# Kernel optimization log

Measured on AMD Instinct MI355X. Metric: run time of the kernel, lower is better.

The kernel has to match this reference:

```python
import math
import jax, jax.numpy as jnp
import numpy as np


def _cirlen(scale):
    # replicates UpSample.get_cirlen: smallest rational period of the scale
    for i in (10, 100, 1000, 10000):
        y = scale * i
        x = i
        if y == math.floor(y):
            break
    y = int(round(y))
    g = math.gcd(x, y)
    return y // g


def _proj(out_len, scale, scale_int, in_len):
    # replicates matmask_made: for each output coord, source coord and repeat index (sca),
    # giving the selected column p = coord*scale_int + sca in the nearest-repeated grid.
    c = np.arange(out_len, dtype=np.float64)
    c[-1] -= 0.1
    coord = np.floor(c / scale).astype(np.int64)
    sca = np.arange(out_len) - np.searchsorted(coord, coord)  # occurrence index per coord
    p = coord * scale_int + sca
    # unfold(kernel=3, dilation=2, padding=2): taps at p-2, p, p+2 in the upscaled grid
    q = p[:, None] + 2 * np.array([-1, 0, 1], dtype=np.int64)[None, :]
    valid = ((q >= 0) & (q < in_len * scale_int)).astype(np.float32)
    src = np.clip(q // scale_int, 0, in_len - 1)  # upscaled pixel q == original pixel q//scale_int
    return src, valid


def reference(x, w1, b1, w2, b2, ln_g, ln_b, scale_x10):
    scale = round(scale_x10 / 10.0, 4)
    scale_int = math.ceil(scale)
    N, C, H, W = x.shape
    outH = math.ceil(scale * H)
    outW = math.ceil(scale * W)
    cycle = _cirlen(scale)
    K = 9 * C

    # ---- per-cycle-position dynamic weights (Scale2Pos_mat + Fea2Weight + LayerNorm) ----
    off = np.arange(cycle, dtype=np.float64) / scale
    off = (off - np.floor(off)).astype(np.float32)
    oh_i, ow_j = np.meshgrid(off, off, indexing='ij')  # row index = i*cycle + j
    posmat = np.stack([np.full_like(oh_i, 1.0 / scale), oh_i, ow_j], axis=-1).reshape(-1, 3)
    posmat = jnp.asarray(posmat)
    h = jax.nn.relu(posmat @ w1 + b1)                       # (cyc^2, 256)
    wflat = h @ w2 + b2                                     # (cyc^2, 9*C*outC)
    outC = wflat.shape[-1] // K
    wv = wflat.reshape(cycle * cycle, outC, K)              # view(pos, outC, K)
    mu = wv.mean(-1, keepdims=True)
    var = wv.var(-1, keepdims=True)                         # biased, as torch LayerNorm
    wv = ((wv - mu) / jnp.sqrt(var + 1e-5)) * ln_g + ln_b
    wv = wv / C
    Wm = jnp.transpose(wv, (0, 2, 1)).reshape(cycle, cycle, K, outC)

    # ---- irregular gather (nearest-repeat + unfold + mask_select), done as direct gather ----
    rs, vh = _proj(outH, scale, scale_int, H)  # (outH,3)
    cs, vw = _proj(outW, scale, scale_int, W)  # (outW,3)
    g = x[:, :, jnp.asarray(rs), :]            # (N,C,outH,3,W)
    g = g[:, :, :, :, jnp.asarray(cs)]         # (N,C,outH,3,outW,3)
    g = g * jnp.asarray(vh)[None, None, :, :, None, None]
    g = g * jnp.asarray(vw)[None, None, None, None, :, :]
    # unfold channel order is (C, kh, kw)
    patch = jnp.transpose(g, (0, 2, 4, 1, 3, 5)).reshape(N, outH, outW, K)

    # ---- pad to cycle multiple, per-cycle-position matmul, crop ----
    Hp = -(-outH // cycle) * cycle
    Wp = -(-outW // cycle) * cycle
    patch = jnp.pad(patch, ((0, 0), (0, Hp - outH), (0, Wp - outW), (0, 0)))
    patch = patch.reshape(N, Hp // cycle, cycle, Wp // cycle, cycle, K)
    out = jnp.einsum('nhiwjk,ijkc->nchiwj', patch, Wm)
    out = out.reshape(N, outC, Hp, Wp)[:, :, :outH, :outW]
    return out


def setup_inputs() -> dict:
    key = jax.random.key(0)
    k = jax.random.split(key, 5)
    inC, outC = 64, 3
    x = jax.random.normal(k[0], (8, inC, 96, 96), dtype=jnp.float32)
    w1 = jax.random.normal(k[1], (3, 256), dtype=jnp.float32) * 0.5
    b1 = jax.random.normal(k[2], (256,), dtype=jnp.float32) * 0.1
    w2 = jax.random.normal(k[3], (256, 9 * inC * outC), dtype=jnp.float32) * 0.0625
    b2 = jax.random.normal(k[4], (9 * inC * outC,), dtype=jnp.float32) * 0.01
    ln_g = jnp.ones((9 * inC,), dtype=jnp.float32)
    ln_b = jnp.zeros((9 * inC,), dtype=jnp.float32)
    return {"x": x, "w1": w1, "b1": b1, "w2": w2, "b2": b2,
            "ln_g": ln_g, "ln_b": ln_b, "scale_x10": 15}
```

## Files before the change

kernel.cpp:

```cpp
#include <hip/hip_runtime.h>
#include <math.h>

#define C_IN   64
#define HW_IN  96
#define N_B    8
#define OUTC   3
#define OUT_HW 144
#define HID    256
#define KDIM   576
#define NFLAT  1728

#define WS_W    0
#define WS_RS   15552
#define WS_VH   15984
#define WS_WF   16416

__global__ __launch_bounds__(256) void a1_wflat(
    const float* __restrict__ w1, const float* __restrict__ b1,
    const float* __restrict__ w2, const float* __restrict__ b2,
    const int* __restrict__ sxp, float* __restrict__ ws)
{
    __shared__ float h[HID];
    __shared__ float part[4 * 64];
    const int cell = blockIdx.x;
    const int tile = blockIdx.y;
    const int tid  = threadIdx.x;

    double scale = (double)sxp[0] / 10.0;
    int ci = cell / 3, cj = cell % 3;
    double oi = (double)ci / scale; oi -= floor(oi);
    double oj = (double)cj / scale; oj -= floor(oj);
    float p0 = (float)(1.0 / scale), p1 = (float)oi, p2 = (float)oj;

    float hv = b1[tid] + p0 * w1[tid] + p1 * w1[HID + tid] + p2 * w1[2 * HID + tid];
    h[tid] = fmaxf(hv, 0.f);
    __syncthreads();

    const int wave = tid >> 6, lane = tid & 63;
    const int col  = tile * 64 + lane;
    const float* w2c = w2 + (size_t)(wave * 64) * NFLAT + col;
    const float* hp  = h + wave * 64;
    float v = 0.f;
    #pragma unroll
    for (int r = 0; r < 64; ++r) v += hp[r] * w2c[(size_t)r * NFLAT];
    part[wave * 64 + lane] = v;
    __syncthreads();

    if (tid < 64) {
        int c2 = tile * 64 + tid;
        float s = b2[c2] + part[tid] + part[64 + tid] + part[128 + tid] + part[192 + tid];
        ws[WS_WF + cell * NFLAT + c2] = s;
    }
}

__global__ __launch_bounds__(256) void a2_ln_pack_proj(
    const float* __restrict__ ln_g, const float* __restrict__ ln_b,
    const int* __restrict__ sxp, float* __restrict__ ws)
{
    __shared__ float rsum[4], rsum2[4];
    const int cell = blockIdx.x, co = blockIdx.y, tid = threadIdx.x;
    const int lane = tid & 63, wid = tid >> 6;

    const float* wfc = ws + WS_WF + cell * NFLAT + co * KDIM;

    float s = 0.f, s2 = 0.f;
    for (int k = tid; k < KDIM; k += 256) { float v = wfc[k]; s += v; s2 += v * v; }
    #pragma unroll
    for (int off = 32; off > 0; off >>= 1) { s += __shfl_down(s, off); s2 += __shfl_down(s2, off); }
    if (lane == 0) { rsum[wid] = s; rsum2[wid] = s2; }
    __syncthreads();
    float S  = rsum[0] + rsum[1] + rsum[2] + rsum[3];
    float Q  = rsum2[0] + rsum2[1] + rsum2[2] + rsum2[3];
    float mu = S * (1.f / KDIM);
    float rstd = rsqrtf(Q * (1.f / KDIM) - mu * mu + 1e-5f);

    for (int k = tid; k < KDIM; k += 256) {
        float v = ((wfc[k] - mu) * rstd * ln_g[k] + ln_b[k]) * (1.f / C_IN);
        int c = k / 9, t = k % 9;
        ws[WS_W + cell * NFLAT + c * 27 + t * 3 + co] = v;
    }

    if (cell == 0 && co == 0 && tid < OUT_HW) {
        double scale = (double)sxp[0] / 10.0;
        int scale_int = (int)ceil(scale - 1e-9);
        double cc = (double)tid; if (tid == OUT_HW - 1) cc -= 0.1;
        long coord = (long)floor(cc / scale);
        long first = (long)ceil((double)coord * scale);
        long p = coord * (long)scale_int + ((long)tid - first);
        #pragma unroll
        for (int d = 0; d < 3; ++d) {
            long q = p + 2 * (d - 1);
            bool ok = (q >= 0) && (q < (long)HW_IN * scale_int);
            long src = (q < 0) ? 0 : q / scale_int;
            if (src > HW_IN - 1) src = HW_IN - 1;
            ws[WS_RS + tid * 3 + d] = (float)src;
            ws[WS_VH + tid * 3 + d] = ok ? 1.f : 0.f;
        }
    }
}

#define JSTRIDE 2056

__global__ __launch_bounds__(192) void c_main(
    const float* __restrict__ x, const float* __restrict__ ws,
    float* __restrict__ out)
{
    __shared__ float Wl[3 * JSTRIDE];
    const int tid = threadIdx.x;
    const int oh  = blockIdx.x;
    const int n0  = blockIdx.y;
    const int i   = oh % 3;

    for (int idx = tid; idx < 3 * 64 * 32; idx += 192) {
        int j = idx >> 11;
        int rem = idx & 2047;
        int c = rem >> 5, m = rem & 31;
        float v = 0.f;
        if (m < 27) v = ws[WS_W + (size_t)((i * 3 + j) * 64 + c) * 27 + m];
        Wl[j * JSTRIDE + c * 32 + m] = v;
    }
    __syncthreads();

    const int ow = tid;
    if (ow >= OUT_HW) return;

    const float* rsf = ws + WS_RS;
    const float* vhf = ws + WS_VH;
    const int jj = ow % 3;
    const float* Wj = Wl + jj * JSTRIDE;

    int s[3]; float vw[3];
    #pragma unroll
    for (int d = 0; d < 3; ++d) { s[d] = (int)rsf[ow * 3 + d]; vw[d] = vhf[ow * 3 + d]; }

    int xoff[9]; float vv[9];
    #pragma unroll
    for (int dr = 0; dr < 3; ++dr) {
        int r = (int)rsf[oh * 3 + dr];
        float vhd = vhf[oh * 3 + dr];
        #pragma unroll
        for (int dc = 0; dc < 3; ++dc) {
            xoff[dr * 3 + dc] = r * HW_IN + s[dc];
            vv[dr * 3 + dc]   = vhd * vw[dc];
        }
    }

    const float* xb0 = x + (size_t)n0 * C_IN * HW_IN * HW_IN;
    const float* xb1 = xb0 + (size_t)4 * C_IN * HW_IN * HW_IN;
    float acc[2][3] = {{0.f,0.f,0.f},{0.f,0.f,0.f}};

    #pragma unroll 2
    for (int c = 0; c < C_IN; ++c) {
        const float* xc0 = xb0 + c * (HW_IN * HW_IN);
        const float* xc1 = xb1 + c * (HW_IN * HW_IN);
        float w[28];
        const float4* wp = (const float4*)(Wj + c * 32);
        #pragma unroll
        for (int q = 0; q < 7; ++q) ((float4*)w)[q] = wp[q];
        #pragma unroll
        for (int t = 0; t < 9; ++t) {
            float xv0 = xc0[xoff[t]] * vv[t];
            float xv1 = xc1[xoff[t]] * vv[t];
            acc[0][0] += xv0 * w[t * 3 + 0];
            acc[0][1] += xv0 * w[t * 3 + 1];
            acc[0][2] += xv0 * w[t * 3 + 2];
            acc[1][0] += xv1 * w[t * 3 + 0];
            acc[1][1] += xv1 * w[t * 3 + 1];
            acc[1][2] += xv1 * w[t * 3 + 2];
        }
    }

    #pragma unroll
    for (int rr = 0; rr < 2; ++rr) {
        int n = n0 + rr * 4;
        #pragma unroll
        for (int co = 0; co < OUTC; ++co)
            out[((size_t)(n * OUTC + co) * OUT_HW + oh) * OUT_HW + ow] = acc[rr][co];
    }
}

extern "C" void kernel_launch(void* const* d_in, const int* in_sizes, int n_in,
                              void* d_out, int out_size, void* d_ws, size_t ws_size,
                              hipStream_t stream)
{
    const float* x    = (const float*)d_in[0];
    const float* w1   = (const float*)d_in[1];
    const float* b1   = (const float*)d_in[2];
    const float* w2   = (const float*)d_in[3];
    const float* b2   = (const float*)d_in[4];
    const float* ln_g = (const float*)d_in[5];
    const float* ln_b = (const float*)d_in[6];
    const int*   sx   = (const int*)d_in[7];
    float* ws  = (float*)d_ws;
    float* out = (float*)d_out;

    a1_wflat<<<dim3(9, 27), 256, 0, stream>>>(w1, b1, w2, b2, sx, ws);
    a2_ln_pack_proj<<<dim3(9, 3), 256, 0, stream>>>(ln_g, ln_b, sx, ws);
    c_main<<<dim3(OUT_HW, 4), 192, 0, stream>>>(x, ws, out);
}
```

Before: 137.8 us.

## Regroup main kernel by cycle phase so each block shares uniform weights

```diff
diff --git a/kernel.cpp b/kernel.cpp
--- a/kernel.cpp
+++ b/kernel.cpp
@@ -99,84 +99,84 @@
     }
 }
 
-#define JSTRIDE 2056
-
-__global__ __launch_bounds__(192) void c_main(
+__global__ __launch_bounds__(256) void c_phase(
     const float* __restrict__ x, const float* __restrict__ ws,
     float* __restrict__ out)
 {
-    __shared__ float Wl[3 * JSTRIDE];
-    const int tid = threadIdx.x;
-    const int oh  = blockIdx.x;
-    const int n0  = blockIdx.y;
-    const int i   = oh % 3;
-
-    for (int idx = tid; idx < 3 * 64 * 32; idx += 192) {
-        int j = idx >> 11;
-        int rem = idx & 2047;
-        int c = rem >> 5, m = rem & 31;
-        float v = 0.f;
-        if (m < 27) v = ws[WS_W + (size_t)((i * 3 + j) * 64 + c) * 27 + m];
-        Wl[j * JSTRIDE + c * 32 + m] = v;
-    }
-    __syncthreads();
-
-    const int ow = tid;
-    if (ow >= OUT_HW) return;
+    const int tid   = threadIdx.x;
+    const int phase = blockIdx.y;
+    const int i  = phase / 3, jj = phase % 3;
+    const int idx = blockIdx.x * 256 + tid;
+    const int ow_idx = idx % 48;
+    const int t2     = idx / 48;
+    const int oh_idx = t2 % 48;
+    const int n      = t2 / 48;
+    const int oh = i  + 3 * oh_idx;
+    const int ow = jj + 3 * ow_idx;
 
     const float* rsf = ws + WS_RS;
     const float* vhf = ws + WS_VH;
-    const int jj = ow % 3;
-    const float* Wj = Wl + jj * JSTRIDE;
 
     int s[3]; float vw[3];
     #pragma unroll
     for (int d = 0; d < 3; ++d) { s[d] = (int)rsf[ow * 3 + d]; vw[d] = vhf[ow * 3 + d]; }
 
-    int xoff[9]; float vv[9];
+    int xoff[9]; float vv[9]; bool interior = true;
     #pragma unroll
     for (int dr = 0; dr < 3; ++dr) {
         int r = (int)rsf[oh * 3 + dr];
         float vhd = vhf[oh * 3 + dr];
         #pragma unroll
         for (int dc = 0; dc < 3; ++dc) {
+            float v = vhd * vw[dc];
             xoff[dr * 3 + dc] = r * HW_IN + s[dc];
-            vv[dr * 3 + dc]   = vhd * vw[dc];
-        }
-    }
-
-    const float* xb0 = x + (size_t)n0 * C_IN * HW_IN * HW_IN;
-    const float* xb1 = xb0 + (size_t)4 * C_IN * HW_IN * HW_IN;
-    float acc[2][3] = {{0.f,0.f,0.f},{0.f,0.f,0.f}};
-
-    #pragma unroll 2
-    for (int c = 0; c < C_IN; ++c) {
-        const float* xc0 = xb0 + c * (HW_IN * HW_IN);
-        const float* xc1 = xb1 + c * (HW_IN * HW_IN);
-        float w[28];
-        const float4* wp = (const float4*)(Wj + c * 32);
-        #pragma unroll
-        for (int q = 0; q < 7; ++q) ((float4*)w)[q] = wp[q];
-        #pragma unroll
-        for (int t = 0; t < 9; ++t) {
-            float xv0 = xc0[xoff[t]] * vv[t];
-            float xv1 = xc1[xoff[t]] * vv[t];
-            acc[0][0] += xv0 * w[t * 3 + 0];
-            acc[0][1] += xv0 * w[t * 3 + 1];
-            acc[0][2] += xv0 * w[t * 3 + 2];
-            acc[1][0] += xv1 * w[t * 3 + 0];
-            acc[1][1] += xv1 * w[t * 3 + 1];
-            acc[1][2] += xv1 * w[t * 3 + 2];
-        }
-    }
-
-    #pragma unroll
-    for (int rr = 0; rr < 2; ++rr) {
-        int n = n0 + rr * 4;
-        #pragma unroll
-        for (int co = 0; co < OUTC; ++co)
-            out[((size_t)(n * OUTC + co) * OUT_HW + oh) * OUT_HW + ow] = acc[rr][co];
-    }
+            vv[dr * 3 + dc]   = v;
+            interior = interior && (v == 1.f);
+        }
+    }
+
+    const float* wcell = ws + WS_W + phase * NFLAT;
+    const float* xc = x + (size_t)n * C_IN * (HW_IN * HW_IN);
+    float a0 = 0.f, a1 = 0.f, a2 = 0.f;
+
+    if (interior) {
+        #pragma unroll 2
+        for (int c = 0; c < C_IN; ++c) {
+            const float* wp = wcell + c * 27;
+            float w[27];
+            #pragma unroll
+            for (int q = 0; q < 27; ++q) w[q] = wp[q];
+            #pragma unroll
+            for (int t = 0; t < 9; ++t) {
+                float xv = xc[xoff[t]];
+                a0 += xv * w[t * 3 + 0];
+                a1 += xv * w[t * 3 + 1];
+                a2 += xv * w[t * 3 + 2];
+            }
+            xc += HW_IN * HW_IN;
+        }
+    } else {
+        #pragma unroll 2
+        for (int c = 0; c < C_IN; ++c) {
+            const float* wp = wcell + c * 27;
+            float w[27];
+            #pragma unroll
+            for (int q = 0; q < 27; ++q) w[q] = wp[q];
+            #pragma unroll
+            for (int t = 0; t < 9; ++t) {
+                float xv = xc[xoff[t]] * vv[t];
+                a0 += xv * w[t * 3 + 0];
+                a1 += xv * w[t * 3 + 1];
+                a2 += xv * w[t * 3 + 2];
+            }
+            xc += HW_IN * HW_IN;
+        }
+    }
+
+    const size_t ob = ((size_t)n * OUTC) * (OUT_HW * OUT_HW) + (size_t)oh * OUT_HW + ow;
+    out[ob]                           = a0;
+    out[ob +     (OUT_HW * OUT_HW)]   = a1;
+    out[ob + 2 * (OUT_HW * OUT_HW)]   = a2;
 }
 
 extern "C" void kernel_launch(void* const* d_in, const int* in_sizes, int n_in,
@@ -196,5 +196,5 @@
 
     a1_wflat<<<dim3(9, 27), 256, 0, stream>>>(w1, b1, w2, b2, sx, ws);
     a2_ln_pack_proj<<<dim3(9, 3), 256, 0, stream>>>(ln_g, ln_b, sx, ws);
-    c_main<<<dim3(OUT_HW, 4), 192, 0, stream>>>(x, ws, out);
-}
+    c_phase<<<dim3(72, 9), 256, 0, stream>>>(x, ws, out);
+}
```

Measured after the change: 160.9 us. 1.17x slower.

## Recast upsample conv as per-phase bf16 MFMA GEMM over padded NHWC input

Applied to the files above, without the earlier changes.

```diff
diff --git a/kernel.cpp b/kernel.cpp
--- a/kernel.cpp
+++ b/kernel.cpp
@@ -10,15 +10,29 @@
 #define KDIM   576
 #define NFLAT  1728
 
+typedef __attribute__((ext_vector_type(8))) short short8;
+typedef __attribute__((ext_vector_type(4))) float f32x4;
+
+#define XP_BYTES   (8u * 98 * 98 * 64 * 2)
+#define WP_OFF     XP_BYTES
+#define WF_OFF     (WP_OFF + 9 * 9216 * 2)
+#define WS_NEED    (WF_OFF + NFLAT * 9 * 4)
+
 #define WS_W    0
 #define WS_RS   15552
 #define WS_VH   15984
 #define WS_WF   16416
 
+__device__ __forceinline__ short f2bf(float f) {
+    unsigned u = __float_as_uint(f);
+    u += 0x7FFFu + ((u >> 16) & 1u);
+    return (short)(u >> 16);
+}
+
 __global__ __launch_bounds__(256) void a1_wflat(
     const float* __restrict__ w1, const float* __restrict__ b1,
     const float* __restrict__ w2, const float* __restrict__ b2,
-    const int* __restrict__ sxp, float* __restrict__ ws)
+    const int* __restrict__ sxp, float* __restrict__ wf)
 {
     __shared__ float h[HID];
     __shared__ float part[4 * 64];
@@ -49,7 +63,123 @@
     if (tid < 64) {
         int c2 = tile * 64 + tid;
         float s = b2[c2] + part[tid] + part[64 + tid] + part[128 + tid] + part[192 + tid];
-        ws[WS_WF + cell * NFLAT + c2] = s;
+        wf[cell * NFLAT + c2] = s;
+    }
+}
+
+__global__ __launch_bounds__(128) void prep_xp(
+    const float* __restrict__ x, short* __restrict__ xp)
+{
+    const int n = blockIdx.x, rp = blockIdx.y, sp = threadIdx.x;
+    if (sp >= 98) return;
+    short8* dst = (short8*)(xp + (((size_t)n * 98 + rp) * 98 + sp) * 64);
+    const bool border = (rp == 0) | (rp == 97) | (sp == 0) | (sp == 97);
+    if (border) {
+        short8 z = {0, 0, 0, 0, 0, 0, 0, 0};
+        #pragma unroll
+        for (int q = 0; q < 8; ++q) dst[q] = z;
+    } else {
+        const float* xs = x + (size_t)n * C_IN * 9216 + (rp - 1) * 96 + (sp - 1);
+        #pragma unroll
+        for (int q = 0; q < 8; ++q) {
+            short8 v;
+            #pragma unroll
+            for (int e = 0; e < 8; ++e)
+                v[e] = f2bf(xs[(size_t)(q * 8 + e) * 9216]);
+            dst[q] = v;
+        }
+    }
+}
+
+__global__ __launch_bounds__(256) void a2_lnW(
+    const float* __restrict__ ln_g, const float* __restrict__ ln_b,
+    const float* __restrict__ wf, short* __restrict__ Wp)
+{
+    __shared__ float rsum[4], rsum2[4];
+    const int cell = blockIdx.x, co = blockIdx.y, tid = threadIdx.x;
+    const int lane = tid & 63, wid = tid >> 6;
+
+    const float* wfc = wf + cell * NFLAT + co * KDIM;
+
+    float s = 0.f, s2 = 0.f;
+    for (int k = tid; k < KDIM; k += 256) { float v = wfc[k]; s += v; s2 += v * v; }
+    #pragma unroll
+    for (int off = 32; off > 0; off >>= 1) { s += __shfl_down(s, off); s2 += __shfl_down(s2, off); }
+    if (lane == 0) { rsum[wid] = s; rsum2[wid] = s2; }
+    __syncthreads();
+    float S  = rsum[0] + rsum[1] + rsum[2] + rsum[3];
+    float Q  = rsum2[0] + rsum2[1] + rsum2[2] + rsum2[3];
+    float mu = S * (1.f / KDIM);
+    float rstd = rsqrtf(Q * (1.f / KDIM) - mu * mu + 1e-5f);
+
+    for (int k = tid; k < KDIM; k += 256) {
+        float v = ((wfc[k] - mu) * rstd * ln_g[k] + ln_b[k]) * (1.f / C_IN);
+        int c = k / 9, t = k - 9 * c;
+        int kp = t * 64 + c;
+        Wp[((size_t)(cell * 72 + (kp >> 3)) * 16 + co) * 8 + (kp & 7)] = f2bf(v);
+    }
+    if (co == 0) {
+        for (int e = tid; e < 72 * 13 * 8; e += 256) {
+            int u = e & 7, r = e >> 3;
+            int colz = 3 + (r % 13), kc = r / 13;
+            Wp[((size_t)(cell * 72 + kc) * 16 + colz) * 8 + u] = 0;
+        }
+    }
+}
+
+__global__ __launch_bounds__(256) void c_mfma(
+    const short* __restrict__ xp, const short* __restrict__ Wp,
+    float* __restrict__ out)
+{
+    __shared__ short Bs[9216];
+    const int tid = threadIdx.x;
+    const int phase = blockIdx.y;
+    const int i = phase / 3, jj = phase % 3;
+
+    {
+        short8* d = (short8*)Bs;
+        const short8* sgl = (const short8*)(Wp + (size_t)phase * 9216);
+        for (int e = tid; e < 1152; e += 256) d[e] = sgl[e];
+    }
+    __syncthreads();
+
+    const int lane = tid & 63, wave = tid >> 6;
+    const int q = lane >> 4;
+
+    const int pix = blockIdx.x * 64 + wave * 16;
+    const int m0 = pix % 48;
+    const int t2 = pix / 48;
+    const int k  = t2 % 48;
+    const int n  = t2 / 48;
+
+    const int di = (i == 2), dj = (jj == 2);
+    const int r0 = 2 * k + di;
+    const int m  = m0 + (lane & 15);
+    const int s0 = 2 * m + dj;
+
+    const short8* A0 = (const short8*)(xp + (((size_t)n * 98 + r0) * 98 + s0) * 64 + q * 8);
+    const short8* A1 = A0 + 98 * 8;
+    const short8* A2 = A0 + 196 * 8;
+    const short8* Bp = (const short8*)Bs + (q * 16 + (lane & 15));
+
+    f32x4 acc = {0.f, 0.f, 0.f, 0.f};
+    #pragma unroll
+    for (int kb = 0; kb < 18; ++kb) {
+        const int t = kb >> 1, dr = t / 3, dc = t % 3;
+        short8 av = (dr == 0 ? A0 : dr == 1 ? A1 : A2)[dc * 8 + (kb & 1) * 4];
+        short8 bv = Bp[kb * 64];
+        acc = __builtin_amdgcn_mfma_f32_16x16x32_bf16(av, bv, acc, 0, 0, 0);
+    }
+
+    const int col = lane & 15;
+    if (col < 3) {
+        const int oh = i + 3 * k;
+        const size_t ob = ((size_t)(n * OUTC + col) * OUT_HW + oh) * OUT_HW;
+        #pragma unroll
+        for (int reg = 0; reg < 4; ++reg) {
+            int mm = m0 + q * 4 + reg;
+            out[ob + jj + 3 * mm] = acc[reg];
+        }
     }
 }
 
@@ -89,9 +219,9 @@
         long p = coord * (long)scale_int + ((long)tid - first);
         #pragma unroll
         for (int d = 0; d < 3; ++d) {
-            long q = p + 2 * (d - 1);
-            bool ok = (q >= 0) && (q < (long)HW_IN * scale_int);
-            long src = (q < 0) ? 0 : q / scale_int;
+            long qq = p + 2 * (d - 1);
+            bool ok = (qq >= 0) && (qq < (long)HW_IN * scale_int);
+            long src = (qq < 0) ? 0 : qq / scale_int;
             if (src > HW_IN - 1) src = HW_IN - 1;
             ws[WS_RS + tid * 3 + d] = (float)src;
             ws[WS_VH + tid * 3 + d] = ok ? 1.f : 0.f;
@@ -100,7 +230,6 @@
 }
 
 #define JSTRIDE 2056
-
 __global__ __launch_bounds__(192) void c_main(
     const float* __restrict__ x, const float* __restrict__ ws,
     float* __restrict__ out)
@@ -108,16 +237,16 @@
     __shared__ float Wl[3 * JSTRIDE];
     const int tid = threadIdx.x;
     const int oh  = blockIdx.x;
-    const int n0  = blockIdx.y;
+    const int n   = blockIdx.y;
     const int i   = oh % 3;
 
     for (int idx = tid; idx < 3 * 64 * 32; idx += 192) {
         int j = idx >> 11;
         int rem = idx & 2047;
-        int c = rem >> 5, m = rem & 31;
+        int c = rem >> 5, mm = rem & 31;
         float v = 0.f;
-        if (m < 27) v = ws[WS_W + (size_t)((i * 3 + j) * 64 + c) * 27 + m];
-        Wl[j * JSTRIDE + c * 32 + m] = v;
+        if (mm < 27) v = ws[WS_W + (size_t)((i * 3 + j) * 64 + c) * 27 + mm];
+        Wl[j * JSTRIDE + c * 32 + mm] = v;
     }
     __syncthreads();
 
@@ -126,8 +255,8 @@
 
     const float* rsf = ws + WS_RS;
     const float* vhf = ws + WS_VH;
-    const int jj = ow % 3;
-    const float* Wj = Wl + jj * JSTRIDE;
+    const int jjf = ow % 3;
+    const float* Wj = Wl + jjf * JSTRIDE;
 
     int s[3]; float vw[3];
     #pragma unroll
@@ -145,38 +274,28 @@
         }
     }
 
-    const float* xb0 = x + (size_t)n0 * C_IN * HW_IN * HW_IN;
-    const float* xb1 = xb0 + (size_t)4 * C_IN * HW_IN * HW_IN;
-    float acc[2][3] = {{0.f,0.f,0.f},{0.f,0.f,0.f}};
+    const float* xb = x + (size_t)n * C_IN * HW_IN * HW_IN;
+    float acc[3] = {0.f, 0.f, 0.f};
 
     #pragma unroll 2
     for (int c = 0; c < C_IN; ++c) {
-        const float* xc0 = xb0 + c * (HW_IN * HW_IN);
-        const float* xc1 = xb1 + c * (HW_IN * HW_IN);
+        const float* xc = xb + c * (HW_IN * HW_IN);
         float w[28];
         const float4* wp = (const float4*)(Wj + c * 32);
         #pragma unroll
-        for (int q = 0; q < 7; ++q) ((float4*)w)[q] = wp[q];
+        for (int qq = 0; qq < 7; ++qq) ((float4*)w)[qq] = wp[qq];
         #pragma unroll
         for (int t = 0; t < 9; ++t) {
-            float xv0 = xc0[xoff[t]] * vv[t];
-            float xv1 = xc1[xoff[t]] * vv[t];
-            acc[0][0] += xv0 * w[t * 3 + 0];
-            acc[0][1] += xv0 * w[t * 3 + 1];
-            acc[0][2] += xv0 * w[t * 3 + 2];
-            acc[1][0] += xv1 * w[t * 3 + 0];
-            acc[1][1] += xv1 * w[t * 3 + 1];
-            acc[1][2] += xv1 * w[t * 3 + 2];
-        }
-    }
-
-    #pragma unroll
-    for (int rr = 0; rr < 2; ++rr) {
-        int n = n0 + rr * 4;
-        #pragma unroll
-        for (int co = 0; co < OUTC; ++co)
-            out[((size_t)(n * OUTC + co) * OUT_HW + oh) * OUT_HW + ow] = acc[rr][co];
-    }
+            float xv = xc[xoff[t]] * vv[t];
+            acc[0] += xv * w[t * 3 + 0];
+            acc[1] += xv * w[t * 3 + 1];
+            acc[2] += xv * w[t * 3 + 2];
+        }
+    }
+
+    #pragma unroll
+    for (int co = 0; co < OUTC; ++co)
+        out[((size_t)(n * OUTC + co) * OUT_HW + oh) * OUT_HW + ow] = acc[co];
 }
 
 extern "C" void kernel_launch(void* const* d_in, const int* in_sizes, int n_in,
@@ -191,10 +310,21 @@
     const float* ln_g = (const float*)d_in[5];
     const float* ln_b = (const float*)d_in[6];
     const int*   sx   = (const int*)d_in[7];
-    float* ws  = (float*)d_ws;
     float* out = (float*)d_out;
-
-    a1_wflat<<<dim3(9, 27), 256, 0, stream>>>(w1, b1, w2, b2, sx, ws);
-    a2_ln_pack_proj<<<dim3(9, 3), 256, 0, stream>>>(ln_g, ln_b, sx, ws);
-    c_main<<<dim3(OUT_HW, 4), 192, 0, stream>>>(x, ws, out);
-}
+    char*  wsb = (char*)d_ws;
+
+    if (ws_size >= (size_t)WS_NEED) {
+        short* xp = (short*)wsb;
+        short* Wp = (short*)(wsb + WP_OFF);
+        float* wf = (float*)(wsb + WF_OFF);
+        a1_wflat<<<dim3(9, 27), 256, 0, stream>>>(w1, b1, w2, b2, sx, wf);
+        prep_xp<<<dim3(8, 98), 128, 0, stream>>>(x, xp);
+        a2_lnW<<<dim3(9, 3), 256, 0, stream>>>(ln_g, ln_b, wf, Wp);
+        c_mfma<<<dim3(288, 9), 256, 0, stream>>>(xp, Wp, out);
+    } else {
+        float* ws = (float*)d_ws;
+        a1_wflat<<<dim3(9, 27), 256, 0, stream>>>(w1, b1, w2, b2, sx, ws + WS_WF);
+        a2_ln_pack_proj<<<dim3(9, 3), 256, 0, stream>>>(ln_g, ln_b, sx, ws);
+        c_main<<<dim3(OUT_HW, N_B), 192, 0, stream>>>(x, ws, out);
+    }
+}
```

Result: faster. 118.7 us (-13.8%).
